# Kernel tuning notes

Hardware: AMD Instinct MI355X
Metric: run time of the kernel (lower is better)

Reference implementation:

```python
import jax, jax.numpy as jnp
import numpy as np
from jax import lax

R = 3                      # blob_r
S = 2 * R + 1              # 7: maxpool / neighborhood kernel size
THRESH = 0.997
PS_XY = 0.1                # vs_xy
PS_Z = 0.02                # vs_z
ZMIN = -2.0                # zrange[0]
K_PEAKS = 131072           # static upper bound replacing torch.nonzero

_offs = np.arange(S)
_gz, _gy, _gx = np.meshgrid(_offs, _offs, _offs, indexing='ij')  # patch axis order [z,y,x]
GZ = jnp.asarray(_gz.ravel(), dtype=jnp.int32)
GY = jnp.asarray(_gy.ravel(), dtype=jnp.int32)
GX = jnp.asarray(_gx.ravel(), dtype=jnp.int32)
# centroid filters: offsets -r..r along the matching patch axis (matches torch meshgrid layout)
FZ = jnp.asarray((_gz.ravel() - R).astype(np.float32))
FY = jnp.asarray((_gy.ravel() - R).astype(np.float32))
FX = jnp.asarray((_gx.ravel() - R).astype(np.float32))


def setup_inputs() -> dict:
    key = jax.random.key(0)
    pred_vol = jax.random.uniform(key, (1, 1, 128, 512, 512), dtype=jnp.float32)
    return {"pred_vol": pred_vol, "max_peaks": K_PEAKS}


def _forward(pred_vol, max_peaks):
    vol = pred_vol[0, 0]                               # [D,H,W]
    D, H, W = vol.shape
    thr = jnp.where(vol > THRESH, vol, 0.0)
    # MaxPool3d(kernel=2r+1, stride=1, padding=r) == SAME max window (pad with -inf)
    mp = lax.reduce_window(thr, -jnp.inf, lax.max, (S, S, S), (1, 1, 1), [(R, R)] * 3)
    conf = jnp.where((mp > 0.0) & (mp == thr), mp, 0.0)  # local maxima above threshold
    # fixed-size peak extraction (replaces torch.nonzero); zero-valued entries are padding
    vals, idx = lax.top_k(conf.reshape(-1), max_peaks)   # [K], [K]
    z = idx // (H * W)
    y = (idx % (H * W)) // W
    x = idx % W
    padv = jnp.pad(vol, R)                               # ConstantPad3d(r, 0)
    # gather (2r+1)^3 neighborhoods around each peak: [K, S^3]
    patches = padv[z[:, None] + GZ[None, :], y[:, None] + GY[None, :], x[:, None] + GX[None, :]]
    s0 = patches.sum(axis=1)                             # conv3d with ones filter == conf_rec sum
    xloc = jnp.einsum('kp,p->k', patches, FX) / s0
    yloc = jnp.einsum('kp,p->k', patches, FY) / s0
    zloc = jnp.einsum('kp,p->k', patches, FZ) / s0
    xf = x.astype(jnp.float32)
    yf = y.astype(jnp.float32)
    zf = z.astype(jnp.float32)
    xrec = (xf + xloc - (W - 1) / 2.0) * PS_XY
    yrec = (yf + yloc - (H - 1) / 2.0) * PS_XY
    zrec = (zf + zloc + 0.5) * PS_Z + ZMIN
    valid = vals > 0.0
    xyz = jnp.where(valid[:, None], jnp.stack((xrec, yrec, zrec), axis=1), 0.0)  # [K,3]
    out = jnp.concatenate([xyz, vals[:, None]], axis=1)  # [K,4] = (x,y,z,conf), padded rows are 0
    return out, valid


def reference(pred_vol, max_peaks):
    return _forward(pred_vol, max_peaks)
```

## Files before the change

### kernel.cpp

```cpp
#include <hip/hip_runtime.h>

#define DD 128
#define HH 512
#define WW 512
#define NVOX (DD*HH*WW)
#define THRESHV 0.997f
#define KPEAKS 131072
#define PEAK_CAP (1u<<18)
#define NBINS 65536


__global__ void k_init(unsigned* counters, unsigned* hist) {
    unsigned t = blockIdx.x * 1024u + threadIdx.x;
    if (t < 64) counters[t] = 0u;
    if (t < NBINS) hist[t] = 0u;
}

__global__ __launch_bounds__(512, 8)
void k_find(const float4* __restrict__ vol4, const float* __restrict__ vol,
            unsigned* counters, unsigned* hist,
            unsigned long long* keys, float4* psums) {
    __shared__ float4 tile[2048];
    __shared__ unsigned lcnt, pcnt, lbase;
    __shared__ unsigned cidx[384];
    __shared__ unsigned long long lbuf[192];
    __shared__ float4 sbuf[192];
    if (threadIdx.x == 0) { lcnt = 0; pcnt = 0; }
    __syncthreads();

    unsigned t = threadIdx.x;
    unsigned lane = t & 63u;
    unsigned w = t >> 6;
    unsigned blockBase4 = blockIdx.x * 2048u;

#pragma unroll
    for (unsigned i = 0; i < 4; i++) {
        unsigned f = i * 512u + w * 64u;
        const float4* gp = vol4 + blockBase4 + f + lane;
        __builtin_amdgcn_global_load_lds(
            (const __attribute__((address_space(1))) unsigned int*)gp,
            (__attribute__((address_space(3))) unsigned int*)(tile + f),
            16, 0, 0);
    }
    __builtin_amdgcn_s_waitcnt(0);
    __syncthreads();

    unsigned m = 0u;
    float4 v[4];
#pragma unroll
    for (unsigned i = 0; i < 4; i++) v[i] = tile[i * 512u + t];
#pragma unroll
    for (unsigned i = 0; i < 4; i++) {
        m |= (v[i].x > THRESHV ? 1u : 0u) << (4 * i);
        m |= (v[i].y > THRESHV ? 1u : 0u) << (4 * i + 1);
        m |= (v[i].z > THRESHV ? 1u : 0u) << (4 * i + 2);
        m |= (v[i].w > THRESHV ? 1u : 0u) << (4 * i + 3);
    }
    while (m) {
        int b = __ffs(m) - 1;
        m &= m - 1u;
        unsigned f4 = blockBase4 + (unsigned)(b >> 2) * 512u + t;
        cidx[atomicAdd(&lcnt, 1u) & 383u] = f4 * 4u + (unsigned)(b & 3);
    }
    __syncthreads();

    unsigned n = lcnt > 384u ? 384u : lcnt;
    int dz = (int)lane / 7, dy = (int)lane - dz * 7;
    for (unsigned base = w * 2u; base < n; base += 16u) {
        bool has2 = (base + 1u < n);
        unsigned idxA = cidx[base];
        unsigned idxB = has2 ? cidx[base + 1u] : idxA;
        int zA = idxA >> 18, yA = (idxA >> 9) & 511, xA = idxA & 511;
        int zB = idxB >> 18, yB = (idxB >> 9) & 511, xB = idxB & 511;
        int nzA = zA + dz - 3, nyA = yA + dy - 3;
        int nzB = zB + dz - 3, nyB = yB + dy - 3;
        bool rowokA = (lane < 49) && ((unsigned)nzA < DD) && ((unsigned)nyA < HH);
        bool rowokB = (lane < 49) && ((unsigned)nzB < DD) && ((unsigned)nyB < HH);
        size_t rbA = rowokA ? (((size_t)(unsigned)nzA << 18) | ((size_t)(unsigned)nyA << 9))
                            : (((size_t)zA << 18) | ((size_t)yA << 9));
        size_t rbB = rowokB ? (((size_t)(unsigned)nzB << 18) | ((size_t)(unsigned)nyB << 9))
                            : (((size_t)zB << 18) | ((size_t)yB << 9));
        float rvA[7], rvB[7];
        bool intAB = (xA >= 3) && (xA <= WW - 4) && (xB >= 3) && (xB <= WW - 4);
        if (intAB) {
            float4 fA0 = *(const float4*)(vol + rbA + (unsigned)(xA - 3));
            float4 fA1 = *(const float4*)(vol + rbA + (unsigned)(xA + 1));
            float4 fB0 = *(const float4*)(vol + rbB + (unsigned)(xB - 3));
            float4 fB1 = *(const float4*)(vol + rbB + (unsigned)(xB + 1));
            rvA[0] = fA0.x; rvA[1] = fA0.y; rvA[2] = fA0.z; rvA[3] = fA0.w;
            rvA[4] = fA1.x; rvA[5] = fA1.y; rvA[6] = fA1.z;
            rvB[0] = fB0.x; rvB[1] = fB0.y; rvB[2] = fB0.z; rvB[3] = fB0.w;
            rvB[4] = fB1.x; rvB[5] = fB1.y; rvB[6] = fB1.z;
        } else {
#pragma unroll
            for (int d = 0; d < 7; d++) {
                int nxA = xA + d - 3;
                bool okA = (unsigned)nxA < WW;
                float va = vol[rbA + (unsigned)(okA ? nxA : xA)];
                rvA[d] = okA ? va : 0.f;
                int nxB = xB + d - 3;
                bool okB = (unsigned)nxB < WW;
                float vb = vol[rbB + (unsigned)(okB ? nxB : xB)];
                rvB[d] = okB ? vb : 0.f;
            }
        }
        if (!rowokA) {
#pragma unroll
            for (int d = 0; d < 7; d++) rvA[d] = 0.f;
        }
        if (!rowokB) {
#pragma unroll
            for (int d = 0; d < 7; d++) rvB[d] = 0.f;
        }
        float centerA = __shfl(rvA[3], 24);
        float centerB = __shfl(rvB[3], 24);

        {
            bool kill = false;
            float s0r = 0.f, sxr = 0.f;
#pragma unroll
            for (int d = 0; d < 7; d++) {
                kill |= rvA[d] > centerA;
                s0r += rvA[d];
                sxr += rvA[d] * (float)(d - 3);
            }
            if (!__any(kill)) {
                float s0 = s0r, sx = sxr;
                float sy = s0r * (float)(dy - 3);
                float sz = s0r * (float)(dz - 3);
                for (int off = 32; off; off >>= 1) {
                    s0 += __shfl_down(s0, off);
                    sx += __shfl_down(sx, off);
                    sy += __shfl_down(sy, off);
                    sz += __shfl_down(sz, off);
                }
                if (lane == 0) {
                    unsigned bits = __float_as_uint(centerA);
                    atomicAdd(&hist[(~bits) & 0xFFFFu], 1u);
                    unsigned li = atomicAdd(&pcnt, 1u);
                    if (li < 192u) {
                        lbuf[li] = ((unsigned long long)bits << 32) | idxA;
                        sbuf[li] = make_float4(s0, sx, sy, sz);
                    }
                }
            }
        }
        if (has2) {
            bool kill = false;
            float s0r = 0.f, sxr = 0.f;
#pragma unroll
            for (int d = 0; d < 7; d++) {
                kill |= rvB[d] > centerB;
                s0r += rvB[d];
                sxr += rvB[d] * (float)(d - 3);
            }
            if (!__any(kill)) {
                float s0 = s0r, sx = sxr;
                float sy = s0r * (float)(dy - 3);
                float sz = s0r * (float)(dz - 3);
                for (int off = 32; off; off >>= 1) {
                    s0 += __shfl_down(s0, off);
                    sx += __shfl_down(sx, off);
                    sy += __shfl_down(sy, off);
                    sz += __shfl_down(sz, off);
                }
                if (lane == 0) {
                    unsigned bits = __float_as_uint(centerB);
                    atomicAdd(&hist[(~bits) & 0xFFFFu], 1u);
                    unsigned li = atomicAdd(&pcnt, 1u);
                    if (li < 192u) {
                        lbuf[li] = ((unsigned long long)bits << 32) | idxB;
                        sbuf[li] = make_float4(s0, sx, sy, sz);
                    }
                }
            }
        }
    }
    __syncthreads();
    if (threadIdx.x == 0) lbase = atomicAdd(&counters[1], pcnt);
    __syncthreads();
    unsigned np = pcnt > 192u ? 192u : pcnt;
    for (unsigned i = threadIdx.x; i < np; i += 512u) {
        unsigned p = lbase + i;
        if (p < PEAK_CAP) { keys[p] = lbuf[i]; psums[p] = sbuf[i]; }
    }
}

__global__ void k_scan(const unsigned* __restrict__ hist, unsigned* cursor) {
    __shared__ unsigned partial[1024];
    int t = threadIdx.x;
    const uint4* h4 = (const uint4*)(hist + t * 64);
    uint4 loc[16];
#pragma unroll
    for (int i = 0; i < 16; i++) loc[i] = h4[i];
    unsigned s = 0;
#pragma unroll
    for (int i = 0; i < 16; i++) s += loc[i].x + loc[i].y + loc[i].z + loc[i].w;
    partial[t] = s;
    __syncthreads();
    for (int off = 1; off < 1024; off <<= 1) {
        unsigned v = (t >= off) ? partial[t - off] : 0u;
        __syncthreads();
        partial[t] += v;
        __syncthreads();
    }
    unsigned run = (t == 0) ? 0u : partial[t - 1];
    uint4* c4 = (uint4*)(cursor + t * 64);
#pragma unroll
    for (int i = 0; i < 16; i++) {
        uint4 h = loc[i]; uint4 o;
        o.x = run; run += h.x;
        o.y = run; run += h.y;
        o.z = run; run += h.z;
        o.w = run; run += h.w;
        c4[i] = o;
    }
}

__global__ void k_scatter(const unsigned* __restrict__ counters,
                          const unsigned long long* __restrict__ keys,
                          unsigned* cursor, unsigned long long* sorted,
                          unsigned* sslot,
                          float4* __restrict__ out, float* __restrict__ valid) {
    unsigned np = counters[1]; if (np > PEAK_CAP) np = PEAK_CAP;
    unsigned t = blockIdx.x * 1024u + threadIdx.x;
    if (t < np) {
        unsigned long long key = keys[t];
        unsigned bits = (unsigned)(key >> 32);
        unsigned pos = atomicAdd(&cursor[(~bits) & 0xFFFFu], 1u);
        if (pos < PEAK_CAP) { sorted[pos] = key; sslot[pos] = t; }
    } else if (t < KPEAKS) {
        out[t] = make_float4(0.f, 0.f, 0.f, 0.f);
        valid[t] = 0.f;
    }
}

__global__ void k_finish(const unsigned* __restrict__ counters,
                         const unsigned long long* __restrict__ sorted,
                         const unsigned* __restrict__ sslot,
                         const float4* __restrict__ psums,
                         float4* __restrict__ out, float* __restrict__ valid) {
    unsigned np = counters[1]; if (np > PEAK_CAP) np = PEAK_CAP;
    unsigned t = blockIdx.x * 1024u + threadIdx.x;
    if (t >= np) return;
    unsigned long long key = sorted[t];
    unsigned bits = (unsigned)(key >> 32);
    unsigned s = t;
    while (s > 0 && (unsigned)(sorted[s - 1] >> 32) == bits) s--;
    unsigned myidx = (unsigned)key;
    unsigned rank = 0, e = s;
    while (e < np) {
        unsigned long long k2 = sorted[e];
        if ((unsigned)(k2 >> 32) != bits) break;
        if ((unsigned)k2 < myidx) rank++;
        e++;
    }
    unsigned row = s + rank;
    if (row >= KPEAKS) return;
    unsigned idx = myidx;
    int z = idx >> 18, y = (idx >> 9) & 511, x = idx & 511;
    float4 ps = psums[sslot[t]];
    float val = __uint_as_float(bits);
    float xloc = ps.y / ps.x, yloc = ps.z / ps.x, zloc = ps.w / ps.x;
    float xr = ((float)x + xloc - (float)(WW - 1) * 0.5f) * 0.1f;
    float yr = ((float)y + yloc - (float)(HH - 1) * 0.5f) * 0.1f;
    float zr = ((float)z + zloc + 0.5f) * 0.02f - 2.0f;
    out[row] = make_float4(xr, yr, zr, val);
    valid[row] = 1.f;
}

extern "C" void kernel_launch(void* const* d_in, const int* in_sizes, int n_in,
                              void* d_out, int out_size, void* d_ws, size_t ws_size,
                              hipStream_t stream) {
    const float* vol = (const float*)d_in[0];

    char* w = (char*)d_ws;
    unsigned* counters = (unsigned*)w;
    unsigned* hist     = (unsigned*)(w + 1024);
    unsigned* cursor   = (unsigned*)(w + 1024 + NBINS * 4);
    char* w2 = w + 1024 + 2 * NBINS * 4;
    unsigned long long* keys   = (unsigned long long*)w2;
    unsigned long long* sorted = keys + PEAK_CAP;
    unsigned* sslot = (unsigned*)(sorted + PEAK_CAP);
    float4*   psums = (float4*)(sslot + PEAK_CAP);

    float* out_rows = (float*)d_out;
    float* valid = out_rows + (size_t)KPEAKS * 4;

    k_init<<<NBINS / 1024, 1024, 0, stream>>>(counters, hist);
    k_find<<<NVOX / 8192, 512, 0, stream>>>((const float4*)vol, vol, counters, hist, keys, psums);
    k_scan<<<1, 1024, 0, stream>>>(hist, cursor);
    k_scatter<<<PEAK_CAP / 1024, 1024, 0, stream>>>(counters, keys, cursor, sorted, sslot,
                                                    (float4*)out_rows, valid);
    k_finish<<<PEAK_CAP / 1024, 1024, 0, stream>>>(counters, sorted, sslot, psums,
                                                   (float4*)out_rows, valid);
}
```

Before: 254.8 us.

## Double-buffer LDS tiles in k_find so each block streams eight tiles

k_find now has each block process eight 1024-float4 tiles through a two-slot LDS ring. The async global-to-LDS load of the next tile is issued while the current tile is thresholded, with explicit vmcnt waits and barriers between stages. The grid shrinks by a factor of four to match. The aim is to hide load latency and amortize per-block setup. In exchange, each block's candidate buffer now covers four times as many voxels, and there are fewer blocks to spread across CUs.

```diff
diff --git a/kernel.cpp b/kernel.cpp
--- a/kernel.cpp
+++ b/kernel.cpp
@@ -9,6 +9,10 @@
 #define PEAK_CAP (1u<<18)
 #define NBINS 65536
 
+#define TILE4 1024u
+#define NT 8u
+#define NBLK (NVOX / (TILE4 * 4u * NT))
+
 
 __global__ void k_init(unsigned* counters, unsigned* hist) {
     unsigned t = blockIdx.x * 1024u + threadIdx.x;
@@ -20,7 +24,7 @@
 void k_find(const float4* __restrict__ vol4, const float* __restrict__ vol,
             unsigned* counters, unsigned* hist,
             unsigned long long* keys, float4* psums) {
-    __shared__ float4 tile[2048];
+    __shared__ float4 tile[2][TILE4];
     __shared__ unsigned lcnt, pcnt, lbase;
     __shared__ unsigned cidx[384];
     __shared__ unsigned long long lbuf[192];
@@ -31,36 +35,55 @@
     unsigned t = threadIdx.x;
     unsigned lane = t & 63u;
     unsigned w = t >> 6;
-    unsigned blockBase4 = blockIdx.x * 2048u;
-
-#pragma unroll
-    for (unsigned i = 0; i < 4; i++) {
-        unsigned f = i * 512u + w * 64u;
-        const float4* gp = vol4 + blockBase4 + f + lane;
-        __builtin_amdgcn_global_load_lds(
-            (const __attribute__((address_space(1))) unsigned int*)gp,
-            (__attribute__((address_space(3))) unsigned int*)(tile + f),
-            16, 0, 0);
-    }
-    __builtin_amdgcn_s_waitcnt(0);
-    __syncthreads();
-
-    unsigned m = 0u;
-    float4 v[4];
-#pragma unroll
-    for (unsigned i = 0; i < 4; i++) v[i] = tile[i * 512u + t];
-#pragma unroll
-    for (unsigned i = 0; i < 4; i++) {
-        m |= (v[i].x > THRESHV ? 1u : 0u) << (4 * i);
-        m |= (v[i].y > THRESHV ? 1u : 0u) << (4 * i + 1);
-        m |= (v[i].z > THRESHV ? 1u : 0u) << (4 * i + 2);
-        m |= (v[i].w > THRESHV ? 1u : 0u) << (4 * i + 3);
-    }
-    while (m) {
-        int b = __ffs(m) - 1;
-        m &= m - 1u;
-        unsigned f4 = blockBase4 + (unsigned)(b >> 2) * 512u + t;
-        cidx[atomicAdd(&lcnt, 1u) & 383u] = f4 * 4u + (unsigned)(b & 3);
+    unsigned blockBase4 = blockIdx.x * (TILE4 * NT);
+
+    auto dma = [&](unsigned tt, unsigned b) {
+#pragma unroll
+        for (unsigned i = 0; i < 2; i++) {
+            unsigned f = i * 512u + w * 64u;
+            const float4* gp = vol4 + blockBase4 + tt * TILE4 + f + lane;
+            __builtin_amdgcn_global_load_lds(
+                (const __attribute__((address_space(1))) unsigned int*)gp,
+                (__attribute__((address_space(3))) unsigned int*)(&tile[b][f]),
+                16, 0, 0);
+        }
+    };
+
+    dma(0u, 0u);
+#pragma unroll
+    for (unsigned tt = 0; tt < NT; tt++) {
+        unsigned b = tt & 1u;
+        if (tt + 1u < NT) {
+            dma(tt + 1u, b ^ 1u);
+            asm volatile("s_waitcnt vmcnt(2)" ::: "memory");
+        } else {
+            asm volatile("s_waitcnt vmcnt(0)" ::: "memory");
+        }
+        __builtin_amdgcn_sched_barrier(0);
+        __builtin_amdgcn_s_barrier();
+        __builtin_amdgcn_sched_barrier(0);
+
+        float4 v0 = tile[b][t];
+        float4 v1 = tile[b][512u + t];
+        unsigned m = 0u;
+        m |= (v0.x > THRESHV ? 1u : 0u);
+        m |= (v0.y > THRESHV ? 2u : 0u);
+        m |= (v0.z > THRESHV ? 4u : 0u);
+        m |= (v0.w > THRESHV ? 8u : 0u);
+        m |= (v1.x > THRESHV ? 16u : 0u);
+        m |= (v1.y > THRESHV ? 32u : 0u);
+        m |= (v1.z > THRESHV ? 64u : 0u);
+        m |= (v1.w > THRESHV ? 128u : 0u);
+        unsigned gbase = blockBase4 + tt * TILE4;
+        while (m) {
+            int bb = __ffs(m) - 1;
+            m &= m - 1u;
+            unsigned f4 = gbase + ((unsigned)bb >> 2) * 512u + t;
+            cidx[atomicAdd(&lcnt, 1u) & 383u] = f4 * 4u + ((unsigned)bb & 3u);
+        }
+        __builtin_amdgcn_sched_barrier(0);
+        __builtin_amdgcn_s_barrier();
+        __builtin_amdgcn_sched_barrier(0);
     }
     __syncthreads();
 
@@ -288,7 +311,7 @@
     float* valid = out_rows + (size_t)KPEAKS * 4;
 
     k_init<<<NBINS / 1024, 1024, 0, stream>>>(counters, hist);
-    k_find<<<NVOX / 8192, 512, 0, stream>>>((const float4*)vol, vol, counters, hist, keys, psums);
+    k_find<<<NBLK, 512, 0, stream>>>((const float4*)vol, vol, counters, hist, keys, psums);
     k_scan<<<1, 1024, 0, stream>>>(hist, cursor);
     k_scatter<<<PEAK_CAP / 1024, 1024, 0, stream>>>(counters, keys, cursor, sorted, sslot,
                                                     (float4*)out_rows, valid);
```

Result: slower. 266.8 us (+4.7%).

## Fuse scan, scatter and finish into one persistent kernel with grid barriers

Applied to the files above, without the earlier changes.

Replaces the single-block histogram scan, the scatter kernel and the finish kernel with one 256-block kernel. The kernel does a two-level parallel scan across blocks and separates its phases with atomic-counter grid barriers. The aim is to remove two kernel launches and the serial one-block scan from the tail. The risk is deadlock if not all 256 blocks of 1024 threads are co-resident. The blocksum array also aliases sslot, which the same kernel overwrites later.

```diff
diff --git a/kernel.cpp b/kernel.cpp
--- a/kernel.cpp
+++ b/kernel.cpp
@@ -8,6 +8,7 @@
 #define KPEAKS 131072
 #define PEAK_CAP (1u<<18)
 #define NBINS 65536
+#define TBLK 256u
 
 
 __global__ void k_init(unsigned* counters, unsigned* hist) {
@@ -186,66 +187,70 @@
     }
 }
 
-__global__ void k_scan(const unsigned* __restrict__ hist, unsigned* cursor) {
-    __shared__ unsigned partial[1024];
-    int t = threadIdx.x;
-    const uint4* h4 = (const uint4*)(hist + t * 64);
-    uint4 loc[16];
-#pragma unroll
-    for (int i = 0; i < 16; i++) loc[i] = h4[i];
-    unsigned s = 0;
-#pragma unroll
-    for (int i = 0; i < 16; i++) s += loc[i].x + loc[i].y + loc[i].z + loc[i].w;
-    partial[t] = s;
-    __syncthreads();
-    for (int off = 1; off < 1024; off <<= 1) {
-        unsigned v = (t >= off) ? partial[t - off] : 0u;
+__device__ __forceinline__ void gbar(unsigned* ctr) {
+    __threadfence();
+    __syncthreads();
+    if (threadIdx.x == 0) {
+        atomicAdd(ctr, 1u);
+        while (atomicAdd(ctr, 0u) < TBLK) {}
+    }
+    __syncthreads();
+    __threadfence();
+}
+
+__global__ __launch_bounds__(1024, 4)
+void k_tail(const unsigned* __restrict__ hist, unsigned* counters,
+            unsigned* cursor, unsigned* blocksum,
+            const unsigned long long* __restrict__ keys,
+            unsigned long long* sorted, unsigned* sslot,
+            const float4* __restrict__ psums,
+            float4* __restrict__ out, float* __restrict__ valid) {
+    __shared__ unsigned sc[256];
+    __shared__ unsigned bs[256];
+    unsigned t = threadIdx.x;
+    unsigned b = blockIdx.x;
+
+    unsigned h = 0u;
+    if (t < 256u) { h = hist[b * 256u + t]; sc[t] = h; }
+    __syncthreads();
+    for (unsigned off = 1u; off < 256u; off <<= 1) {
+        unsigned v = (t < 256u && t >= off) ? sc[t - off] : 0u;
         __syncthreads();
-        partial[t] += v;
+        if (t < 256u) sc[t] += v;
         __syncthreads();
     }
-    unsigned run = (t == 0) ? 0u : partial[t - 1];
-    uint4* c4 = (uint4*)(cursor + t * 64);
-#pragma unroll
-    for (int i = 0; i < 16; i++) {
-        uint4 h = loc[i]; uint4 o;
-        o.x = run; run += h.x;
-        o.y = run; run += h.y;
-        o.z = run; run += h.z;
-        o.w = run; run += h.w;
-        c4[i] = o;
-    }
-}
-
-__global__ void k_scatter(const unsigned* __restrict__ counters,
-                          const unsigned long long* __restrict__ keys,
-                          unsigned* cursor, unsigned long long* sorted,
-                          unsigned* sslot,
-                          float4* __restrict__ out, float* __restrict__ valid) {
+    if (t == 255u) blocksum[b] = sc[255];
+    gbar(&counters[8]);
+
+    if (t < 256u) bs[t] = blocksum[t];
+    __syncthreads();
+    for (unsigned off = 1u; off < 256u; off <<= 1) {
+        unsigned v = (t < 256u && t >= off) ? bs[t - off] : 0u;
+        __syncthreads();
+        if (t < 256u) bs[t] += v;
+        __syncthreads();
+    }
+    unsigned base_b = (b > 0u) ? bs[b - 1u] : 0u;
+    if (t < 256u) cursor[b * 256u + t] = base_b + sc[t] - h;
+    gbar(&counters[9]);
+
     unsigned np = counters[1]; if (np > PEAK_CAP) np = PEAK_CAP;
-    unsigned t = blockIdx.x * 1024u + threadIdx.x;
-    if (t < np) {
-        unsigned long long key = keys[t];
+    unsigned g = b * 1024u + t;
+    if (g < np) {
+        unsigned long long key = keys[g];
         unsigned bits = (unsigned)(key >> 32);
         unsigned pos = atomicAdd(&cursor[(~bits) & 0xFFFFu], 1u);
-        if (pos < PEAK_CAP) { sorted[pos] = key; sslot[pos] = t; }
-    } else if (t < KPEAKS) {
-        out[t] = make_float4(0.f, 0.f, 0.f, 0.f);
-        valid[t] = 0.f;
-    }
-}
-
-__global__ void k_finish(const unsigned* __restrict__ counters,
-                         const unsigned long long* __restrict__ sorted,
-                         const unsigned* __restrict__ sslot,
-                         const float4* __restrict__ psums,
-                         float4* __restrict__ out, float* __restrict__ valid) {
-    unsigned np = counters[1]; if (np > PEAK_CAP) np = PEAK_CAP;
-    unsigned t = blockIdx.x * 1024u + threadIdx.x;
-    if (t >= np) return;
-    unsigned long long key = sorted[t];
+        if (pos < PEAK_CAP) { sorted[pos] = key; sslot[pos] = g; }
+    } else if (g < KPEAKS) {
+        out[g] = make_float4(0.f, 0.f, 0.f, 0.f);
+        valid[g] = 0.f;
+    }
+    gbar(&counters[10]);
+
+    if (g >= np) return;
+    unsigned long long key = sorted[g];
     unsigned bits = (unsigned)(key >> 32);
-    unsigned s = t;
+    unsigned s = g;
     while (s > 0 && (unsigned)(sorted[s - 1] >> 32) == bits) s--;
     unsigned myidx = (unsigned)key;
     unsigned rank = 0, e = s;
@@ -259,7 +264,7 @@
     if (row >= KPEAKS) return;
     unsigned idx = myidx;
     int z = idx >> 18, y = (idx >> 9) & 511, x = idx & 511;
-    float4 ps = psums[sslot[t]];
+    float4 ps = psums[sslot[g]];
     float val = __uint_as_float(bits);
     float xloc = ps.y / ps.x, yloc = ps.z / ps.x, zloc = ps.w / ps.x;
     float xr = ((float)x + xloc - (float)(WW - 1) * 0.5f) * 0.1f;
@@ -284,14 +289,14 @@
     unsigned* sslot = (unsigned*)(sorted + PEAK_CAP);
     float4*   psums = (float4*)(sslot + PEAK_CAP);
 
+    unsigned* blocksum = sslot;
+
     float* out_rows = (float*)d_out;
     float* valid = out_rows + (size_t)KPEAKS * 4;
 
     k_init<<<NBINS / 1024, 1024, 0, stream>>>(counters, hist);
     k_find<<<NVOX / 8192, 512, 0, stream>>>((const float4*)vol, vol, counters, hist, keys, psums);
-    k_scan<<<1, 1024, 0, stream>>>(hist, cursor);
-    k_scatter<<<PEAK_CAP / 1024, 1024, 0, stream>>>(counters, keys, cursor, sorted, sslot,
-                                                    (float4*)out_rows, valid);
-    k_finish<<<PEAK_CAP / 1024, 1024, 0, stream>>>(counters, sorted, sslot, psums,
-                                                   (float4*)out_rows, valid);
-}
+    k_tail<<<TBLK, 1024, 0, stream>>>(hist, counters, cursor, blocksum, keys,
+                                      sorted, sslot, psums,
+                                      (float4*)out_rows, valid);
+}
```

New measurement: 649.6 us. +154.9%, slower.
